# Kernel optimization log

Measured on AMD Instinct MI355X. Metric: run time of the kernel, lower is better.

## Reference

```python
import jax, jax.numpy as jnp
import numpy as np

NUM_STREAM = 4
SINKHORN_ITERS = 20
HC_EPS = 1e-06
NORM_EPS = 1e-06


def sinkhorn_knopps(h, iters, eps):
    # h: [B, S, ns, ns]
    h = jax.nn.softmax(h, axis=-1) + eps
    h = h / (h.sum(-2, keepdims=True) + eps)
    for _ in range(iters - 1):  # fixed small trip count (19), unrolled
        h = h / (h.sum(-1, keepdims=True) + eps)
        h = h / (h.sum(-2, keepdims=True) + eps)
    return h


def setup_inputs() -> dict:
    key = jax.random.key(0)
    k1, k2, k3, k4 = jax.random.split(key, 4)
    B, S, ns, H = 4, 2048, NUM_STREAM, 1024
    mix_hc = (2 + ns) * ns  # 24
    x = jax.random.normal(k1, (B, S, ns, H), dtype=jnp.float32)
    hc_fn = jax.random.normal(k2, (mix_hc, ns * H), dtype=jnp.float32) * 0.02
    hc_scale = jax.random.uniform(k3, (3,), dtype=jnp.float32)
    hc_base = jax.random.normal(k4, (mix_hc,), dtype=jnp.float32)
    return {"x": x, "hc_fn": hc_fn, "hc_scale": hc_scale, "hc_base": hc_base}


def reference(x, hc_fn, hc_scale, hc_base):
    B, S, ns, H = x.shape
    xf = x.reshape(B, S, ns * H).astype(jnp.float32)
    # RMSNorm stats (applied as a post-scale on the linear output, as in source)
    rsqrt = jax.lax.rsqrt(jnp.mean(jnp.square(xf), axis=-1, keepdims=True) + NORM_EPS)
    weight = jnp.einsum('bsd,md->bsm', xf, hc_fn) * rsqrt  # [B, S, mix_hc]
    h_pre = weight[..., :ns]
    h_post = weight[..., ns:2 * ns]
    h_res = weight[..., 2 * ns:].reshape(B, S, ns, ns)
    h_pre = jax.nn.sigmoid(h_pre * hc_scale[0] + hc_base[:ns][None, None, :]) + HC_EPS
    h_post = 2.0 * jax.nn.sigmoid(h_post * hc_scale[1] + hc_base[ns:2 * ns][None, None, :])
    h_res = h_res * hc_scale[2] + hc_base[2 * ns:].reshape(ns, ns)[None, None, :, :]
    h_res = sinkhorn_knopps(h_res, SINKHORN_ITERS, HC_EPS)
    xs = xf.reshape(B, S, ns, H)
    # hc_pre: mix streams into a single vector per token
    y = jnp.einsum('bsn,bsnh->bsh', h_pre, xs)  # [B, S, H]
    # hc_post: broadcast gated y back to streams + Sinkhorn-mixed residual streams
    out = h_post[..., None] * y[:, :, None, :] + jnp.einsum('bsij,bsih->bsjh', h_res, xs)
    return out.astype(x.dtype)
```

## Files before the change

### kernel.cpp

```cpp
#include <hip/hip_runtime.h>
#include <math.h>

#define NS 4
#define HDIM 1024
#define DDIM 4096
#define MT 16
#define KCH 512
#define NKC 8
#define HC_EPS_F 1e-6f
#define NORM_EPS_F 1e-6f

typedef __attribute__((ext_vector_type(8))) short short8;
typedef __attribute__((ext_vector_type(4))) float f32x4;

__device__ __forceinline__ float frcp(float v) { return __builtin_amdgcn_rcpf(v); }

#define CVT_PAIR(j, f0, f1)                                                     \
  { unsigned p0 = __float_as_uint(f0), p1 = __float_as_uint(f1);                \
    H.u[j] = (p1 & 0xFFFF0000u) | (p0 >> 16);                                   \
    unsigned q0 = __float_as_uint((f0) - __uint_as_float(p0 & 0xFFFF0000u));    \
    unsigned q1 = __float_as_uint((f1) - __uint_as_float(p1 & 0xFFFF0000u));    \
    L.u[j] = (q1 & 0xFFFF0000u) | (q0 >> 16); }

__device__ __forceinline__ void cvt_hl(const float4 a, const float4 b,
                                       short8& hi, short8& lo) {
  union { unsigned u[4]; short8 s; } H, L;
  CVT_PAIR(0, a.x, a.y)
  CVT_PAIR(1, a.z, a.w)
  CVT_PAIR(2, b.x, b.y)
  CVT_PAIR(3, b.z, b.w)
  hi = H.s; lo = L.s;
}

__launch_bounds__(256, 1)
__global__ void mhc_dots_mfma(const float* __restrict__ x,
                              const float* __restrict__ hc_fn,
                              float* __restrict__ wp, int ntok) {
  const int lane = threadIdx.x & 63;
  const int wave = threadIdx.x >> 6;
  const int wunit = blockIdx.x * 4 + wave;
  const int mt = wunit >> 3;
  const int kc = wunit & 7;
  const long long tok0 = (long long)mt * MT;
  const int k0 = kc * KCH;

  const int row = lane & 15;
  const int ks  = lane >> 4;

  const float4* ap  = (const float4*)(x + (tok0 + row) * DDIM + k0) + ks * 2;
  const float4* bp0 = (const float4*)(hc_fn + (long long)row * DDIM + k0) + ks * 2;
  const int fr1c = (row < 8) ? (16 + row) : 23;
  const float4* bp1 = (const float4*)(hc_fn + (long long)fr1c * DDIM + k0) + ks * 2;
  const bool v1 = (row < 8);
  const float4 z4 = {0.f, 0.f, 0.f, 0.f};

  f32x4 acc0 = {0.f, 0.f, 0.f, 0.f};
  f32x4 acc1 = {0.f, 0.f, 0.f, 0.f};
  float ssq = 0.f;

  float4 a0_c = ap[0], a1_c = ap[1];
  float4 b00_c = bp0[0], b01_c = bp0[1];
  float4 b10_c = v1 ? bp1[0] : z4, b11_c = v1 ? bp1[1] : z4;
  float4 a0_n = ap[8], a1_n = ap[9];
  float4 b00_n = bp0[8], b01_n = bp0[9];
  float4 b10_n = v1 ? bp1[8] : z4, b11_n = v1 ? bp1[9] : z4;

  #pragma unroll 4
  for (int s = 0; s < KCH / 32; ++s) {
    float4 a0_p, a1_p, b00_p, b01_p, b10_p, b11_p;
    if (s < 14) {
      const int o = (s + 2) * 8;
      a0_p = ap[o]; a1_p = ap[o + 1];
      b00_p = bp0[o]; b01_p = bp0[o + 1];
      b10_p = v1 ? bp1[o] : z4; b11_p = v1 ? bp1[o + 1] : z4;
    }

    ssq = fmaf(a0_c.x, a0_c.x, fmaf(a0_c.y, a0_c.y, fmaf(a0_c.z, a0_c.z, fmaf(a0_c.w, a0_c.w, ssq))));
    ssq = fmaf(a1_c.x, a1_c.x, fmaf(a1_c.y, a1_c.y, fmaf(a1_c.z, a1_c.z, fmaf(a1_c.w, a1_c.w, ssq))));

    short8 ahi, alo, b0hi, b0lo, b1hi, b1lo;
    cvt_hl(a0_c, a1_c, ahi, alo);
    cvt_hl(b00_c, b01_c, b0hi, b0lo);
    cvt_hl(b10_c, b11_c, b1hi, b1lo);

    acc0 = __builtin_amdgcn_mfma_f32_16x16x32_bf16(ahi, b0hi, acc0, 0, 0, 0);
    acc1 = __builtin_amdgcn_mfma_f32_16x16x32_bf16(ahi, b1hi, acc1, 0, 0, 0);
    acc0 = __builtin_amdgcn_mfma_f32_16x16x32_bf16(ahi, b0lo, acc0, 0, 0, 0);
    acc1 = __builtin_amdgcn_mfma_f32_16x16x32_bf16(ahi, b1lo, acc1, 0, 0, 0);
    acc0 = __builtin_amdgcn_mfma_f32_16x16x32_bf16(alo, b0hi, acc0, 0, 0, 0);
    acc1 = __builtin_amdgcn_mfma_f32_16x16x32_bf16(alo, b1hi, acc1, 0, 0, 0);

    if (s < 15) {
      a0_c = a0_n; a1_c = a1_n;
      b00_c = b00_n; b01_c = b01_n;
      b10_c = b10_n; b11_c = b11_n;
    }
    if (s < 14) {
      a0_n = a0_p; a1_n = a1_p;
      b00_n = b00_p; b01_n = b01_p;
      b10_n = b10_p; b11_n = b11_p;
    }
  }

  ssq += __shfl_xor(ssq, 16, 64);
  ssq += __shfl_xor(ssq, 32, 64);

  float* wpk = wp + (long long)kc * ntok * 25;
  if (lane < 16) wpk[(tok0 + lane) * 25 + 24] = ssq;
  const int rq = lane >> 4;
  #pragma unroll
  for (int r = 0; r < 4; ++r)
    wpk[(tok0 + rq * 4 + r) * 25 + row] = acc0[r];
  if (row < 8) {
    #pragma unroll
    for (int r = 0; r < 4; ++r)
      wpk[(tok0 + rq * 4 + r) * 25 + 16 + row] = acc1[r];
  }
}

__launch_bounds__(256, 4)
__global__ void mhc_sinkhorn(const float* __restrict__ wp,
                             const float* __restrict__ hc_scale,
                             const float* __restrict__ hc_base,
                             float* __restrict__ gates, int ntok) {
  const int lane = threadIdx.x & 63;
  const int wave = threadIdx.x >> 6;
  const long long tok = (long long)blockIdx.x * 16 + wave * 4 + (lane >> 4);
  const int e = lane & 15;

  const long long kstride = (long long)ntok * 25;
  const float* b = wp + tok * 25;
  float sres = 0.f, ssq = 0.f, spre = 0.f, spost = 0.f;
  #pragma unroll
  for (int kc = 0; kc < NKC; ++kc) {
    const float* p = b + kc * kstride;
    sres += p[8 + e];
    ssq  += p[24];
    if (e < NS) { spre += p[e]; spost += p[NS + e]; }
  }

  const float rs = rsqrtf(ssq * (1.0f / DDIM) + NORM_EPS_F);
  const float s0 = hc_scale[0], s1 = hc_scale[1], s2 = hc_scale[2];

  float h = sres * rs * s2 + hc_base[8 + e];
  float mx = fmaxf(h, __shfl_xor(h, 1, 4));
  mx = fmaxf(mx, __shfl_xor(mx, 2, 4));
  float ex = expf(h - mx);
  float sm = ex + __shfl_xor(ex, 1, 4);
  sm += __shfl_xor(sm, 2, 4);
  h = ex * frcp(sm) + HC_EPS_F;
  float cs = h + __shfl_xor(h, 4, 16);
  cs += __shfl_xor(cs, 8, 16);
  h *= frcp(cs + HC_EPS_F);
  #pragma unroll 1
  for (int itn = 0; itn < 19; ++itn) {
    float rsum = h + __shfl_xor(h, 1, 4);
    rsum += __shfl_xor(rsum, 2, 4);
    h *= frcp(rsum + HC_EPS_F);
    float csum = h + __shfl_xor(h, 4, 16);
    csum += __shfl_xor(csum, 8, 16);
    h *= frcp(csum + HC_EPS_F);
  }
  float* g = gates + tok * 24;
  g[8 + e] = h;
  if (e < NS) {
    g[e] = frcp(1.0f + expf(-(spre * rs * s0 + hc_base[e]))) + HC_EPS_F;
    g[NS + e] = 2.0f * frcp(1.0f + expf(-(spost * rs * s1 + hc_base[NS + e])));
  }
}

__launch_bounds__(256, 8)
__global__ void mhc_out(const float* __restrict__ x,
                        const float* __restrict__ gates,
                        float* __restrict__ out) {
  const long long token = blockIdx.x;
  const int q = threadIdx.x;

  const float* g = gates + token * 24;
  float hp[NS], hq[NS], hr[NS][NS];
  #pragma unroll
  for (int i = 0; i < NS; ++i) {
    hp[i] = g[i];
    hq[i] = g[NS + i];
    #pragma unroll
    for (int j = 0; j < NS; ++j) hr[i][j] = g[8 + i * NS + j];
  }

  const float4* xb = (const float4*)(x + token * DDIM);
  float4 xv[NS];
  #pragma unroll
  for (int i = 0; i < NS; ++i) xv[i] = xb[i * 256 + q];

  float4 y;
  y.x = hp[0]*xv[0].x + hp[1]*xv[1].x + hp[2]*xv[2].x + hp[3]*xv[3].x;
  y.y = hp[0]*xv[0].y + hp[1]*xv[1].y + hp[2]*xv[2].y + hp[3]*xv[3].y;
  y.z = hp[0]*xv[0].z + hp[1]*xv[1].z + hp[2]*xv[2].z + hp[3]*xv[3].z;
  y.w = hp[0]*xv[0].w + hp[1]*xv[1].w + hp[2]*xv[2].w + hp[3]*xv[3].w;

  float4* ob = (float4*)(out + token * DDIM);
  #pragma unroll
  for (int n = 0; n < NS; ++n) {
    float4 o;
    o.x = hq[n]*y.x + hr[0][n]*xv[0].x + hr[1][n]*xv[1].x + hr[2][n]*xv[2].x + hr[3][n]*xv[3].x;
    o.y = hq[n]*y.y + hr[0][n]*xv[0].y + hr[1][n]*xv[1].y + hr[2][n]*xv[2].y + hr[3][n]*xv[3].y;
    o.z = hq[n]*y.z + hr[0][n]*xv[0].z + hr[1][n]*xv[1].z + hr[2][n]*xv[2].z + hr[3][n]*xv[3].z;
    o.w = hq[n]*y.w + hr[0][n]*xv[0].w + hr[1][n]*xv[1].w + hr[2][n]*xv[2].w + hr[3][n]*xv[3].w;
    ob[n * 256 + q] = o;
  }
}

extern "C" void kernel_launch(void* const* d_in, const int* in_sizes, int n_in,
                              void* d_out, int out_size, void* d_ws, size_t ws_size,
                              hipStream_t stream) {
  const float* x        = (const float*)d_in[0];
  const float* hc_fn    = (const float*)d_in[1];
  const float* hc_scale = (const float*)d_in[2];
  const float* hc_base  = (const float*)d_in[3];
  float* out = (float*)d_out;

  const int ntok = in_sizes[0] / DDIM;
  float* gates = (float*)d_ws;
  float* wp    = out;

  const int wave_units = (ntok / MT) * NKC;
  mhc_dots_mfma<<<wave_units / 4, 256, 0, stream>>>(x, hc_fn, wp, ntok);
  mhc_sinkhorn<<<ntok / 16, 256, 0, stream>>>(wp, hc_scale, hc_base, gates, ntok);
  mhc_out<<<ntok, 256, 0, stream>>>(x, gates, out);
}
```

Before: 95.18 us.

## Stage x tiles into LDS via direct global-to-LDS loads in dots kernel

The dot-product kernel now stages each block's 32-token by 512-column slice of x into shared memory with global_load_lds. Four waves split that tile into two token halves and two K halves, which doubles the partial-sum slices the Sinkhorn kernel must reduce (16 instead of 8). The aim is to replace per-wave register prefetch of x with bulk asynchronous loads and to raise occupancy to two blocks per CU. The cost is 64KB of LDS per block, a barrier, more partial-sum traffic, and the loss of the software prefetch for the A operand.

```diff
diff --git a/kernel.cpp b/kernel.cpp
--- a/kernel.cpp
+++ b/kernel.cpp
@@ -4,9 +4,9 @@
 #define NS 4
 #define HDIM 1024
 #define DDIM 4096
-#define MT 16
+#define TOK_B 32
 #define KCH 512
-#define NKC 8
+#define NPS 16
 #define HC_EPS_F 1e-6f
 #define NORM_EPS_F 1e-6f
 
@@ -14,6 +14,12 @@
 typedef __attribute__((ext_vector_type(4))) float f32x4;
 
 __device__ __forceinline__ float frcp(float v) { return __builtin_amdgcn_rcpf(v); }
+
+__device__ __forceinline__ void gload_lds16(const float* g, float* l) {
+  __builtin_amdgcn_global_load_lds(
+      (const __attribute__((address_space(1))) void*)g,
+      (__attribute__((address_space(3))) void*)l, 16, 0, 0);
+}
 
 #define CVT_PAIR(j, f0, f1)                                                     \
   { unsigned p0 = __float_as_uint(f0), p1 = __float_as_uint(f1);                \
@@ -32,25 +38,35 @@
   hi = H.s; lo = L.s;
 }
 
-__launch_bounds__(256, 1)
+__launch_bounds__(256, 2)
 __global__ void mhc_dots_mfma(const float* __restrict__ x,
                               const float* __restrict__ hc_fn,
                               float* __restrict__ wp, int ntok) {
-  const int lane = threadIdx.x & 63;
-  const int wave = threadIdx.x >> 6;
-  const int wunit = blockIdx.x * 4 + wave;
-  const int mt = wunit >> 3;
-  const int kc = wunit & 7;
-  const long long tok0 = (long long)mt * MT;
+  __shared__ float xs[TOK_B * KCH];
+  const int tid  = threadIdx.x;
+  const int lane = tid & 63;
+  const int wave = tid >> 6;
+  const int mt = blockIdx.x >> 3;
+  const int kc = blockIdx.x & 7;
+  const long long tok0 = (long long)mt * TOK_B;
   const int k0 = kc * KCH;
 
+  #pragma unroll
+  for (int c = 0; c < 16; ++c) {
+    const int S = c * 256 + wave * 64;
+    const int t = S >> 7;
+    const int b = (S & 127) + lane;
+    gload_lds16(x + (tok0 + t) * DDIM + k0 + b * 4, xs + (size_t)S * 4);
+  }
+
+  const int th = wave & 1;
+  const int kh = wave >> 1;
   const int row = lane & 15;
   const int ks  = lane >> 4;
 
-  const float4* ap  = (const float4*)(x + (tok0 + row) * DDIM + k0) + ks * 2;
-  const float4* bp0 = (const float4*)(hc_fn + (long long)row * DDIM + k0) + ks * 2;
+  const float4* bp0 = (const float4*)(hc_fn + (long long)row * DDIM + k0 + kh * 256) + ks * 2;
   const int fr1c = (row < 8) ? (16 + row) : 23;
-  const float4* bp1 = (const float4*)(hc_fn + (long long)fr1c * DDIM + k0) + ks * 2;
+  const float4* bp1 = (const float4*)(hc_fn + (long long)fr1c * DDIM + k0 + kh * 256) + ks * 2;
   const bool v1 = (row < 8);
   const float4 z4 = {0.f, 0.f, 0.f, 0.f};
 
@@ -58,28 +74,29 @@
   f32x4 acc1 = {0.f, 0.f, 0.f, 0.f};
   float ssq = 0.f;
 
-  float4 a0_c = ap[0], a1_c = ap[1];
   float4 b00_c = bp0[0], b01_c = bp0[1];
   float4 b10_c = v1 ? bp1[0] : z4, b11_c = v1 ? bp1[1] : z4;
-  float4 a0_n = ap[8], a1_n = ap[9];
-  float4 b00_n = bp0[8], b01_n = bp0[9];
-  float4 b10_n = v1 ? bp1[8] : z4, b11_n = v1 ? bp1[9] : z4;
-
-  #pragma unroll 4
-  for (int s = 0; s < KCH / 32; ++s) {
-    float4 a0_p, a1_p, b00_p, b01_p, b10_p, b11_p;
-    if (s < 14) {
-      const int o = (s + 2) * 8;
-      a0_p = ap[o]; a1_p = ap[o + 1];
-      b00_p = bp0[o]; b01_p = bp0[o + 1];
-      b10_p = v1 ? bp1[o] : z4; b11_p = v1 ? bp1[o + 1] : z4;
+
+  __syncthreads();
+
+  const float* a_base = xs + (size_t)(th * 16 + row) * KCH + kh * 256 + ks * 8;
+
+  #pragma unroll
+  for (int s = 0; s < 8; ++s) {
+    float4 b00_n, b01_n, b10_n, b11_n;
+    if (s < 7) {
+      const int o = (s + 1) * 8;
+      b00_n = bp0[o]; b01_n = bp0[o + 1];
+      b10_n = v1 ? bp1[o] : z4; b11_n = v1 ? bp1[o + 1] : z4;
     }
-
-    ssq = fmaf(a0_c.x, a0_c.x, fmaf(a0_c.y, a0_c.y, fmaf(a0_c.z, a0_c.z, fmaf(a0_c.w, a0_c.w, ssq))));
-    ssq = fmaf(a1_c.x, a1_c.x, fmaf(a1_c.y, a1_c.y, fmaf(a1_c.z, a1_c.z, fmaf(a1_c.w, a1_c.w, ssq))));
+    const float4 a0 = *(const float4*)(a_base + s * 32);
+    const float4 a1 = *(const float4*)(a_base + s * 32 + 4);
+
+    ssq = fmaf(a0.x, a0.x, fmaf(a0.y, a0.y, fmaf(a0.z, a0.z, fmaf(a0.w, a0.w, ssq))));
+    ssq = fmaf(a1.x, a1.x, fmaf(a1.y, a1.y, fmaf(a1.z, a1.z, fmaf(a1.w, a1.w, ssq))));
 
     short8 ahi, alo, b0hi, b0lo, b1hi, b1lo;
-    cvt_hl(a0_c, a1_c, ahi, alo);
+    cvt_hl(a0, a1, ahi, alo);
     cvt_hl(b00_c, b01_c, b0hi, b0lo);
     cvt_hl(b10_c, b11_c, b1hi, b1lo);
 
@@ -90,31 +107,27 @@
     acc0 = __builtin_amdgcn_mfma_f32_16x16x32_bf16(alo, b0hi, acc0, 0, 0, 0);
     acc1 = __builtin_amdgcn_mfma_f32_16x16x32_bf16(alo, b1hi, acc1, 0, 0, 0);
 
-    if (s < 15) {
-      a0_c = a0_n; a1_c = a1_n;
+    if (s < 7) {
       b00_c = b00_n; b01_c = b01_n;
       b10_c = b10_n; b11_c = b11_n;
     }
-    if (s < 14) {
-      a0_n = a0_p; a1_n = a1_p;
-      b00_n = b00_p; b01_n = b01_p;
-      b10_n = b10_p; b11_n = b11_p;
-    }
   }
 
   ssq += __shfl_xor(ssq, 16, 64);
   ssq += __shfl_xor(ssq, 32, 64);
 
-  float* wpk = wp + (long long)kc * ntok * 25;
-  if (lane < 16) wpk[(tok0 + lane) * 25 + 24] = ssq;
+  const int ps = kc * 2 + kh;
+  float* wpk = wp + (long long)ps * ntok * 25;
+  const long long tbase = tok0 + th * 16;
+  if (lane < 16) wpk[(tbase + lane) * 25 + 24] = ssq;
   const int rq = lane >> 4;
   #pragma unroll
   for (int r = 0; r < 4; ++r)
-    wpk[(tok0 + rq * 4 + r) * 25 + row] = acc0[r];
+    wpk[(tbase + rq * 4 + r) * 25 + row] = acc0[r];
   if (row < 8) {
     #pragma unroll
     for (int r = 0; r < 4; ++r)
-      wpk[(tok0 + rq * 4 + r) * 25 + 16 + row] = acc1[r];
+      wpk[(tbase + rq * 4 + r) * 25 + 16 + row] = acc1[r];
   }
 }
 
@@ -132,8 +145,8 @@
   const float* b = wp + tok * 25;
   float sres = 0.f, ssq = 0.f, spre = 0.f, spost = 0.f;
   #pragma unroll
-  for (int kc = 0; kc < NKC; ++kc) {
-    const float* p = b + kc * kstride;
+  for (int ps = 0; ps < NPS; ++ps) {
+    const float* p = b + ps * kstride;
     sres += p[8 + e];
     ssq  += p[24];
     if (e < NS) { spre += p[e]; spost += p[NS + e]; }
@@ -222,8 +235,7 @@
   float* gates = (float*)d_ws;
   float* wp    = out;
 
-  const int wave_units = (ntok / MT) * NKC;
-  mhc_dots_mfma<<<wave_units / 4, 256, 0, stream>>>(x, hc_fn, wp, ntok);
+  mhc_dots_mfma<<<(ntok / TOK_B) * 8, 256, 0, stream>>>(x, hc_fn, wp, ntok);
   mhc_sinkhorn<<<ntok / 16, 256, 0, stream>>>(wp, hc_scale, hc_base, gates, ntok);
   mhc_out<<<ntok, 256, 0, stream>>>(x, gates, out);
 }
```

Result: slower. 99.84 us (+4.9%).
